# Optimization experiments

Measured on AMD Instinct MI355X. Metric: run time of the kernel, lower is better.

The kernel has to match this reference:

```python
import jax, jax.numpy as jnp
import numpy as np

H = 128      # hidden_channels
G = 512      # number of graphs in the batch
NEG_SLOPE = 0.2


def _seg_sum(x, idx, n):
    return jax.ops.segment_sum(x, idx, num_segments=n)


def _sage(x_src, x_dst, ei, Wl, bl, Wr):
    # PyG SAGEConv: lin_l(mean_j x_j) + lin_r(x_i); lin_l has bias, lin_r does not.
    s, d = ei[0], ei[1]
    n = x_dst.shape[0]
    agg = _seg_sum(x_src[s], d, n)
    cnt = _seg_sum(jnp.ones((ei.shape[1],), x_src.dtype), d, n)
    mean = agg / jnp.maximum(cnt, 1.0)[:, None]
    return mean @ Wl + bl + x_dst @ Wr


def _gat(x_src, x_dst, ei, Ws, Wd, a_s, a_d, b):
    # PyG GATConv (heads=1, add_self_loops=False, bipartite): segment softmax over dst.
    s, d = ei[0], ei[1]
    n = x_dst.shape[0]
    hs = x_src @ Ws                                  # [N_src, H]
    hd = x_dst @ Wd                                  # [N_dst, H]
    logit = jax.nn.leaky_relu((hs @ a_s)[s] + (hd @ a_d)[d], NEG_SLOPE)
    m = jax.ops.segment_max(logit, d, num_segments=n)
    e = jnp.exp(logit - m[d])
    z = _seg_sum(e, d, n)
    alpha = e / jnp.maximum(z[d], 1e-16)
    return _seg_sum(alpha[:, None] * hs[s], d, n) + b


def _gcn(x, ei, W, b):
    # PyG GCNConv with add_self_loops=True, normalize=True (same src/dst node type).
    s, d = ei[0], ei[1]
    n = x.shape[0]
    deg = _seg_sum(jnp.ones((ei.shape[1],), x.dtype), d, n) + 1.0  # +1 self loop
    dis = jax.lax.rsqrt(deg)
    h = x @ W
    norm = dis[s] * dis[d]
    out = _seg_sum(norm[:, None] * h[s], d, n) + (dis * dis)[:, None] * h
    return out + b


def _pool(x, b):
    s = _seg_sum(x, b, G)
    c = _seg_sum(jnp.ones((x.shape[0],), x.dtype), b, G)
    return s / jnp.maximum(c, 1.0)[:, None]


def setup_inputs() -> dict:
    key = jax.random.key(0)
    ks = iter(jax.random.split(key, 80))
    scale = 1.0 / np.sqrt(H)

    def nrm(shape, sc=scale):
        return jax.random.normal(next(ks), shape, jnp.float32) * sc

    def edges(e, n_src, n_dst):
        src = jax.random.randint(next(ks), (e,), 0, n_src, jnp.int32)
        dst = jax.random.randint(next(ks), (e,), 0, n_dst, jnp.int32)
        return jnp.stack([src, dst])

    def batch(n):
        return jnp.sort(jax.random.randint(next(ks), (n,), 0, G, jnp.int32))

    N_CD, N_SEQ, N_ANNO, N_RANGE, N_MD = 100000, 80000, 80000, 80000, 50000
    inp = {
        'x_cd': nrm((N_CD, H), 1.0), 'x_seq': nrm((N_SEQ, H), 1.0),
        'x_anno': nrm((N_ANNO, H), 1.0), 'x_range': nrm((N_RANGE, H), 1.0),
        'x_md': nrm((N_MD, H), 1.0),
        'ei_seq': edges(160000, N_CD, N_SEQ),
        'ei_anno': edges(200000, N_CD, N_ANNO),
        'ei_range': edges(200000, N_CD, N_RANGE),
        'ei_comp': edges(300000, N_MD, N_CD),
        'ei_cc': edges(300000, N_CD, N_CD),
        'ei_mm': edges(150000, N_MD, N_MD),
        'b_cd': batch(N_CD), 'b_seq': batch(N_SEQ), 'b_anno': batch(N_ANNO),
        'b_range': batch(N_RANGE), 'b_md': batch(N_MD),
    }
    # per-layer stacked params (leading axis = 2 layers)
    for nm, shp in [('Wsl_seq', (2, H, H)), ('bs_seq', (2, H)), ('Wsr_seq', (2, H, H)),
                    ('Wsl_anno', (2, H, H)), ('bs_anno', (2, H)), ('Wsr_anno', (2, H, H)),
                    ('Wg_comp_s', (2, H, H)), ('Wg_comp_d', (2, H, H)),
                    ('ag_comp_s', (2, H)), ('ag_comp_d', (2, H)), ('bg_comp', (2, H)),
                    ('Wg_range_s', (2, H, H)), ('Wg_range_d', (2, H, H)),
                    ('ag_range_s', (2, H)), ('ag_range_d', (2, H)), ('bg_range', (2, H)),
                    ('Wc_cc', (2, H, H)), ('bc_cc', (2, H)),
                    ('Wc_mm', (2, H, H)), ('bc_mm', (2, H)),
                    ('lin1_W', (5 * H, H)), ('lin1_b', (H,)),
                    ('lin2_W', (H, 1)), ('lin2_b', (1,))]:
        inp[nm] = nrm(shp)
    return inp


def reference(x_cd, x_seq, x_anno, x_range, x_md,
              ei_seq, ei_anno, ei_range, ei_comp, ei_cc, ei_mm,
              b_cd, b_seq, b_anno, b_range, b_md,
              Wsl_seq, bs_seq, Wsr_seq, Wsl_anno, bs_anno, Wsr_anno,
              Wg_comp_s, Wg_comp_d, ag_comp_s, ag_comp_d, bg_comp,
              Wg_range_s, Wg_range_d, ag_range_s, ag_range_d, bg_range,
              Wc_cc, bc_cc, Wc_mm, bc_mm,
              lin1_W, lin1_b, lin2_W, lin2_b):
    for l in range(2):
        # HeteroConv aggr='sum': CD receives GAT(MD->CD) + GCN(CD->CD)
        n_cd = (_gat(x_md, x_cd, ei_comp, Wg_comp_s[l], Wg_comp_d[l],
                     ag_comp_s[l], ag_comp_d[l], bg_comp[l])
                + _gcn(x_cd, ei_cc, Wc_cc[l], bc_cc[l]))
        n_seq = _sage(x_cd, x_seq, ei_seq, Wsl_seq[l], bs_seq[l], Wsr_seq[l])
        n_anno = _sage(x_cd, x_anno, ei_anno, Wsl_anno[l], bs_anno[l], Wsr_anno[l])
        n_range = _gat(x_cd, x_range, ei_range, Wg_range_s[l], Wg_range_d[l],
                       ag_range_s[l], ag_range_d[l], bg_range[l])
        n_md = _gcn(x_md, ei_mm, Wc_mm[l], bc_mm[l])
        x_cd, x_seq, x_anno, x_range, x_md = (
            jax.nn.relu(n_cd), jax.nn.relu(n_seq), jax.nn.relu(n_anno),
            jax.nn.relu(n_range), jax.nn.relu(n_md))
    emb = jnp.concatenate([_pool(x_cd, b_cd), _pool(x_seq, b_seq),
                           _pool(x_anno, b_anno), _pool(x_range, b_range),
                           _pool(x_md, b_md)], axis=-1)        # [G, 5H]
    h = jax.nn.relu(emb @ lin1_W + lin1_b)  # Dropout(0.7) is identity in eval
    return (h @ lin2_W + lin2_b).reshape(-1)  # [G]
```

## Files before the change

### kernel.cpp

```cpp
#include <hip/hip_runtime.h>

#define HD 128
#define GNUM 512
#define RPB 520
#define IDXCAP 512
#define TM 32

typedef __attribute__((ext_vector_type(8))) short short8v;
typedef __attribute__((ext_vector_type(4))) float f32x4;

__device__ __forceinline__ void split1(float a, short& h, short& l) {
  unsigned u = __float_as_uint(a);
  unsigned hb = (u + 0x7FFFu + ((u >> 16) & 1u)) & 0xFFFF0000u;
  h = (short)(hb >> 16);
  float rest = a - __uint_as_float(hb);
  unsigned u2 = __float_as_uint(rest);
  l = (short)((u2 + 0x7FFFu + ((u2 >> 16) & 1u)) >> 16);
}

struct WTab { const float* p[8]; };
__global__ __launch_bounds__(256) void k_split_w(WTab tab, short* __restrict__ whi,
                                                 short* __restrict__ wlo)
{
  int m = blockIdx.x >> 6;
  int i = (blockIdx.x & 63) * 256 + threadIdx.x;
  const float* W = tab.p[m >> 1] + (m & 1) * 16384;
  int k = i >> 7, n = i & 127;
  short h, l;
  split1(W[k * 128 + n], h, l);
  whi[m * 16384 + n * 128 + k] = h;
  wlo[m * 16384 + n * 128 + k] = l;
}

struct COp {
  const float* A; const short* WH; const short* WL;
  const int* grp; const int* gcol;
  const float* wsrc; const float* rowsc; int mode;
};
#define CF_LD 132
__global__ __launch_bounds__(256) void k_gemm_conv(
    COp o0, COp o1, int hasO1,
    float* __restrict__ C, const float* __restrict__ bias, const float* __restrict__ bias2,
    int N, int relu,
    const float* __restrict__ avec, float* __restrict__ adot,
    const float* __restrict__ avec2, float* __restrict__ adot2,
    const int* __restrict__ bvec, float* __restrict__ poolbuf, int coloff)
{
  __shared__ char smem[TM * 136 * 2 * 2];
  __shared__ int idxbuf[IDXCAP];
  __shared__ float wbuf[IDXCAP];
  __shared__ int bsh[TM];
  short* Ah = (short*)smem;
  short* Al = Ah + TM * 136;
  float* Cf = (float*)smem;

  const int t = threadIdx.x;
  const int row0 = blockIdx.x * TM;
  const int lane = t & 63, wid = t >> 6;
  const int g = lane >> 4, cn = lane & 15;
  const int colbase = wid * 32;

  f32x4 zero = {0.f, 0.f, 0.f, 0.f};
  f32x4 acc[2][2];
#pragma unroll
  for (int rt = 0; rt < 2; ++rt) { acc[rt][0] = zero; acc[rt][1] = zero; }

  auto storeAhl = [&](int row, int ln, float4 s) {
    short4 h, l;
    split1(s.x, h.x, l.x); split1(s.y, h.y, l.y);
    split1(s.z, h.z, l.z); split1(s.w, h.w, l.w);
    *(short4*)(Ah + row * 136 + ln * 4) = h;
    *(short4*)(Al + row * 136 + ln * 4) = l;
  };

  auto stageA = [&](const float* __restrict__ A) {
#pragma unroll
    for (int i = 0; i < 4; ++i) {
      int f4 = t + i * 256;
      int row = f4 >> 5, c4 = f4 & 31;
      float4 v = make_float4(0.f, 0.f, 0.f, 0.f);
      if (row0 + row < N) v = ((const float4*)(A + (size_t)row0 * 128))[f4];
      storeAhl(row, c4, v);
    }
  };

  auto prefetch = [&](const COp& op) {
    const int row_end = min(row0 + TM, N);
    const int e_lo = op.grp[row0];
    const int cnt = min(op.grp[row_end] - e_lo, IDXCAP);
    for (int k = t; k < cnt; k += 256) {
      int idx = op.gcol[e_lo + k];
      idxbuf[k] = idx;
      if (op.wsrc) wbuf[k] = op.wsrc[idx];
    }
  };

  auto stage_gather = [&](const COp& op) {
    const int e_lo = op.grp[row0];
    const int mode = op.mode;
    const float* X = op.A;
    auto getcw = [&](int e, int& c, float& w) {
      int off = e - e_lo;
      if (off < IDXCAP) { c = idxbuf[off]; w = wbuf[off]; }
      else { c = op.gcol[e]; w = op.wsrc ? op.wsrc[c] : 0.f; }
    };
#pragma unroll
    for (int i = 0; i < 8; ++i) {
      int f = t + i * 256;
      int row = f >> 6;
      int ln = f & 31;
      int half = (f >> 5) & 1;
      int r = row0 + row;
      float4 s = make_float4(0.f, 0.f, 0.f, 0.f);
      int e0 = 0, e1 = 0;
      float rs = 0.f;
      if (r < N) {
        e0 = op.grp[r]; e1 = op.grp[r + 1];
        if (mode >= 2) rs = op.rowsc[r];
      }
      float z = 0.f;
      if (mode == 2 && half == 0 && r < N) {
        float4 xs_ = *(const float4*)(X + (size_t)r * 128 + ln * 4);
        float rr = rs * rs;
        s.x = rr * xs_.x; s.y = rr * xs_.y; s.z = rr * xs_.z; s.w = rr * xs_.w;
      }
      for (int e = e0 + half; e < e1; e += 2) {
        int c; float w;
        getcw(e, c, w);
        float p;
        if (mode == 3) {
          float v = w + rs; v = v > 0.f ? v : 0.2f * v;
          p = __expf(v); z += p;
        } else if (mode == 2) p = w * rs;
        else p = 1.f;
        float4 a = *(const float4*)(X + (size_t)c * 128 + ln * 4);
        s.x += p * a.x; s.y += p * a.y; s.z += p * a.z; s.w += p * a.w;
      }
      s.x += __shfl_xor(s.x, 32); s.y += __shfl_xor(s.y, 32);
      s.z += __shfl_xor(s.z, 32); s.w += __shfl_xor(s.w, 32);
      if (mode == 3) z += __shfl_xor(z, 32);
      if (half == 0) {
        if (mode == 1) {
          float inv = 1.f / fmaxf((float)(e1 - e0), 1.f);
          s.x *= inv; s.y *= inv; s.z *= inv; s.w *= inv;
        } else if (mode == 3) {
          float inv = (e1 > e0) ? 1.f / z : 0.f;
          s.x *= inv; s.y *= inv; s.z *= inv; s.w *= inv;
        }
        storeAhl(row, ln, s);
      }
    }
  };

  auto accum = [&](const short* __restrict__ WH, const short* __restrict__ WL) {
#pragma unroll
    for (int kg = 0; kg < 4; ++kg) {
      short8v bhi[2], blo[2];
#pragma unroll
      for (int ct = 0; ct < 2; ++ct) {
        size_t o = (size_t)(colbase + ct * 16 + cn) * 128 + kg * 32 + g * 8;
        bhi[ct] = *(const short8v*)(WH + o);
        blo[ct] = *(const short8v*)(WL + o);
      }
#pragma unroll
      for (int rt = 0; rt < 2; ++rt) {
        const int ao = (rt * 16 + cn) * 136 + kg * 32 + g * 8;
        const short8v ah = *(const short8v*)(Ah + ao);
        const short8v al = *(const short8v*)(Al + ao);
#pragma unroll
        for (int ct = 0; ct < 2; ++ct) {
          acc[rt][ct] = __builtin_amdgcn_mfma_f32_16x16x32_bf16(ah, bhi[ct], acc[rt][ct], 0, 0, 0);
          acc[rt][ct] = __builtin_amdgcn_mfma_f32_16x16x32_bf16(al, bhi[ct], acc[rt][ct], 0, 0, 0);
          acc[rt][ct] = __builtin_amdgcn_mfma_f32_16x16x32_bf16(ah, blo[ct], acc[rt][ct], 0, 0, 0);
        }
      }
    }
  };

  if (o0.mode) {
    prefetch(o0);
    __syncthreads();
    stage_gather(o0);
  } else {
    stageA(o0.A);
  }
  __syncthreads();
  if (hasO1 && o1.mode) prefetch(o1);
  accum(o0.WH, o0.WL);
  if (hasO1) {
    __syncthreads();
    if (o1.mode) stage_gather(o1); else stageA(o1.A);
    __syncthreads();
    accum(o1.WH, o1.WL);
  }
  __syncthreads();

#pragma unroll
  for (int rt = 0; rt < 2; ++rt)
#pragma unroll
    for (int ct = 0; ct < 2; ++ct)
#pragma unroll
      for (int r = 0; r < 4; ++r)
        Cf[(rt * 16 + g * 4 + r) * CF_LD + colbase + ct * 16 + cn] = acc[rt][ct][r];
  __syncthreads();

  float4* C4 = C ? (float4*)(C + (size_t)row0 * 128) : nullptr;
#pragma unroll
  for (int i = 0; i < 4; ++i) {
    int f4 = t + i * 256;
    int row = f4 >> 5, c4 = f4 & 31;
    if (row0 + row < N) {
      float4 v = *(const float4*)(Cf + row * CF_LD + c4 * 4);
      if (bias) {
        float4 bv = *(const float4*)(bias + c4 * 4);
        v.x += bv.x; v.y += bv.y; v.z += bv.z; v.w += bv.w;
      }
      if (bias2) {
        float4 bv = *(const float4*)(bias2 + c4 * 4);
        v.x += bv.x; v.y += bv.y; v.z += bv.z; v.w += bv.w;
      }
      if (relu) {
        v.x = fmaxf(v.x, 0.f); v.y = fmaxf(v.y, 0.f);
        v.z = fmaxf(v.z, 0.f); v.w = fmaxf(v.w, 0.f);
      }
      if (C) C4[f4] = v;
      *(float4*)(Cf + row * CF_LD + c4 * 4) = v;
      if (avec) {
        float4 av = *(const float4*)(avec + c4 * 4);
        float p = v.x * av.x + v.y * av.y + v.z * av.z + v.w * av.w;
#pragma unroll
        for (int o = 1; o < 32; o <<= 1) p += __shfl_xor(p, o);
        if (c4 == 0) adot[row0 + row] = p;
      }
      if (avec2) {
        float4 av = *(const float4*)(avec2 + c4 * 4);
        float p = v.x * av.x + v.y * av.y + v.z * av.z + v.w * av.w;
#pragma unroll
        for (int o = 1; o < 32; o <<= 1) p += __shfl_xor(p, o);
        if (c4 == 0) adot2[row0 + row] = p;
      }
    }
  }

  if (poolbuf) {
    if (t < TM) { int r = row0 + t; bsh[t] = (r < N) ? bvec[r] : -1; }
    __syncthreads();
    if (t < 128) {
      int c = t;
      float sum = 0.f;
      int cur = bsh[0];
      for (int r = 0; r < TM; ++r) {
        int gg = bsh[r];
        if (gg < 0) break;
        if (gg != cur) {
          atomicAdd(poolbuf + (size_t)cur * 640 + coloff + c, sum);
          sum = 0.f; cur = gg;
        }
        sum += Cf[r * CF_LD + c];
      }
      if (cur >= 0) atomicAdd(poolbuf + (size_t)cur * 640 + coloff + c, sum);
    }
  }
}

__global__ void k_rowdot(const float* __restrict__ x, const float* __restrict__ a,
                         float* __restrict__ out, int N)
{
  int wid = blockIdx.x * 4 + (threadIdx.x >> 6);
  int lane = threadIdx.x & 63;
  if (wid >= N) return;
  float2 xv = ((const float2*)x)[(size_t)wid * 64 + lane];
  float2 av = ((const float2*)a)[lane];
  float v = fmaf(xv.y, av.y, xv.x * av.x);
#pragma unroll
  for (int o = 32; o > 0; o >>= 1) v += __shfl_down(v, o);
  if (lane == 0) out[wid] = v;
}

__global__ void k_rowdot2(const float* __restrict__ x, const float* __restrict__ a1,
                          const float* __restrict__ a2, float* __restrict__ o1,
                          float* __restrict__ o2, int N)
{
  int wid = blockIdx.x * 4 + (threadIdx.x >> 6);
  int lane = threadIdx.x & 63;
  if (wid >= N) return;
  float2 xv = ((const float2*)x)[(size_t)wid * 64 + lane];
  float2 av1 = ((const float2*)a1)[lane];
  float2 av2 = ((const float2*)a2)[lane];
  float v1 = fmaf(xv.y, av1.y, xv.x * av1.x);
  float v2 = fmaf(xv.y, av2.y, xv.x * av2.x);
#pragma unroll
  for (int o = 32; o > 0; o >>= 1) { v1 += __shfl_down(v1, o); v2 += __shfl_down(v2, o); }
  if (lane == 0) { o1[wid] = v1; o2[wid] = v2; }
}

struct MTab { const float* W[8]; const float* a[8]; };
__global__ __launch_bounds__(128) void k_matvec8(MTab tb, float* __restrict__ wv)
{
  __shared__ float as[128];
  int m = blockIdx.x, i = threadIdx.x;
  as[i] = tb.a[m][i];
  __syncthreads();
  const float* W = tb.W[m];
  float v = 0.f;
  for (int j = 0; j < 128; ++j) v = fmaf(W[i * 128 + j], as[j], v);
  wv[m * 128 + i] = v;
}

struct HTab { const int* key[6]; int* cnt[6]; unsigned short* rank[6]; int bo[7]; int n[6]; };
__global__ void k_hist_rank_all(HTab tb) {
  int bi = blockIdx.x, ty = 0;
  while (ty < 5 && bi >= tb.bo[ty + 1]) ++ty;
  int i = (bi - tb.bo[ty]) * 256 + threadIdx.x;
  if (i < tb.n[ty])
    tb.rank[ty][i] = (unsigned short)atomicAdd(&tb.cnt[ty][tb.key[ty][i]], 1);
}

struct FTab { const int* es[6]; const int* ed[6]; const int* rp[6];
              const unsigned short* rank[6]; int* col[6]; int bo[7]; int n[6]; };
__global__ void k_fill_all(FTab tb) {
  int bi = blockIdx.x, ty = 0;
  while (ty < 5 && bi >= tb.bo[ty + 1]) ++ty;
  int e = (bi - tb.bo[ty]) * 256 + threadIdx.x;
  if (e >= tb.n[ty]) return;
  int p = tb.rp[ty][tb.ed[ty][e]] + (int)tb.rank[ty][e];
  tb.col[ty][p] = tb.es[ty][e];
}

struct STab { int* rp[6]; int* bs[6]; int n[6]; int bo[7]; };

__global__ __launch_bounds__(256) void k_scan_partial_all(STab tb) {
  __shared__ int red[256];
  int bi = blockIdx.x, ty = 0;
  while (ty < 5 && bi >= tb.bo[ty + 1]) ++ty;
  int lb = bi - tb.bo[ty];
  const int* rp = tb.rp[ty];
  const int N = tb.n[ty];
  const int t = threadIdx.x, base = lb * 4096;
  int s = 0;
  for (int i = t; i < 4096; i += 256) {
    int idx = base + i;
    if (idx < N) s += rp[idx];
  }
  red[t] = s;
  __syncthreads();
  for (int ofs = 128; ofs > 0; ofs >>= 1) {
    if (t < ofs) red[t] += red[t + ofs];
    __syncthreads();
  }
  if (t == 0) tb.bs[ty][lb] = red[0];
}

__global__ __launch_bounds__(256) void k_scan_bsums_all(STab tb) {
  __shared__ int sh[256];
  const int ty = blockIdx.x;
  const int nb = (tb.n[ty] + 4095) / 4096;
  const int t = threadIdx.x;
  int v = (t < nb) ? tb.bs[ty][t] : 0;
  sh[t] = v;
  __syncthreads();
  for (int ofs = 1; ofs < 256; ofs <<= 1) {
    int u = (t >= ofs) ? sh[t - ofs] : 0;
    __syncthreads();
    sh[t] += u;
    __syncthreads();
  }
  if (t < nb) tb.bs[ty][t] = sh[t] - v;
  if (t == 255) tb.rp[ty][tb.n[ty]] = sh[255];
}

__global__ __launch_bounds__(256) void k_scan_final_all(STab tb) {
  __shared__ int sh[4096 + 256];
  __shared__ int tsum[256];
  int bi = blockIdx.x, ty = 0;
  while (ty < 5 && bi >= tb.bo[ty + 1]) ++ty;
  int lb = bi - tb.bo[ty];
  int* rp = tb.rp[ty];
  const int N = tb.n[ty];
  const int t = threadIdx.x, base = lb * 4096;
  auto mp = [](int i) { return i + (i >> 4); };
#pragma unroll
  for (int i = 0; i < 16; ++i) {
    int idx = base + i * 256 + t;
    sh[mp(i * 256 + t)] = (idx < N) ? rp[idx] : 0;
  }
  __syncthreads();
  int s = 0;
#pragma unroll
  for (int j = 0; j < 16; ++j) s += sh[mp(t * 16 + j)];
  tsum[t] = s;
  __syncthreads();
  for (int ofs = 1; ofs < 256; ofs <<= 1) {
    int u = (t >= ofs) ? tsum[t - ofs] : 0;
    __syncthreads();
    tsum[t] += u;
    __syncthreads();
  }
  int pre = tsum[t] - s + tb.bs[ty][lb];
#pragma unroll
  for (int j = 0; j < 16; ++j) {
    int v = sh[mp(t * 16 + j)];
    sh[mp(t * 16 + j)] = pre;
    pre += v;
  }
  __syncthreads();
#pragma unroll
  for (int i = 0; i < 16; ++i) {
    int idx = base + i * 256 + t;
    if (idx < N) rp[idx] = sh[mp(i * 256 + t)];
  }
}

struct BTab { const int* b[5]; int n[5]; };
__global__ __launch_bounds__(512) void k_runptr(BTab tb, int* __restrict__ rpb_all) {
  const int ty = blockIdx.x;
  const int* b = tb.b[ty];
  const int N = tb.n[ty];
  const int t = threadIdx.x;
  int lo = 0, hi = N;
  while (lo < hi) {
    int mid = (lo + hi) >> 1;
    if (b[mid] < t) lo = mid + 1; else hi = mid;
  }
  rpb_all[ty * RPB + t] = lo;
  if (t == 0) rpb_all[ty * RPB + GNUM] = N;
}

struct DTab { const int* rp[2]; float* dis[2]; int n[2]; int bo[3]; };
__global__ void k_dis2(DTab tb) {
  int bi = blockIdx.x, ty = (bi >= tb.bo[1]) ? 1 : 0;
  int n = (bi - tb.bo[ty]) * 256 + threadIdx.x;
  if (n < tb.n[ty]) tb.dis[ty][n] = rsqrtf((float)(tb.rp[ty][n + 1] - tb.rp[ty][n]) + 1.f);
}

__global__ void k_mlp(const float* __restrict__ pool, const int* __restrict__ rpb_all,
                      const float* __restrict__ W1, const float* __restrict__ b1,
                      const float* __restrict__ W2, const float* __restrict__ b2,
                      float* __restrict__ out)
{
  __shared__ float emb[640];
  __shared__ float red[128];
  const int g = blockIdx.x, t = threadIdx.x;
  for (int i = t; i < 640; i += 128) {
    int type = i >> 7;
    int cnt = rpb_all[type * RPB + g + 1] - rpb_all[type * RPB + g];
    emb[i] = pool[(size_t)g * 640 + i] / fmaxf((float)cnt, 1.f);
  }
  __syncthreads();
  float acc = b1[t];
  for (int i = 0; i < 640; ++i) acc = fmaf(emb[i], W1[i * 128 + t], acc);
  float h = fmaxf(acc, 0.f);
  red[t] = h * W2[t];
  __syncthreads();
  for (int s = 64; s > 0; s >>= 1) {
    if (t < s) red[t] += red[t + s];
    __syncthreads();
  }
  if (t == 0) out[g] = red[0] + b2[0];
}

extern "C" void kernel_launch(void* const* d_in, const int* in_sizes, int n_in,
                              void* d_out, int out_size, void* d_ws, size_t ws_size,
                              hipStream_t stream)
{
  auto fin = [&](int i) { return (const float*)d_in[i]; };
  auto iin = [&](int i) { return (const int*)d_in[i]; };

  const float *x_cd = fin(0), *x_seq = fin(1), *x_anno = fin(2), *x_range = fin(3), *x_md = fin(4);
  const int *ei_seq = iin(5), *ei_anno = iin(6), *ei_range = iin(7),
            *ei_comp = iin(8), *ei_cc = iin(9), *ei_mm = iin(10);
  const int *b_cd = iin(11), *b_seq = iin(12), *b_anno = iin(13), *b_range = iin(14), *b_md = iin(15);

  const int N_CD = in_sizes[0] / HD, N_SEQ = in_sizes[1] / HD, N_ANNO = in_sizes[2] / HD,
            N_RANGE = in_sizes[3] / HD, N_MD = in_sizes[4] / HD;
  const int E_seq = in_sizes[5] / 2, E_anno = in_sizes[6] / 2, E_range = in_sizes[7] / 2,
            E_comp = in_sizes[8] / 2, E_cc = in_sizes[9] / 2, E_mm = in_sizes[10] / 2;
  const int N_OTH = max(max(N_SEQ, N_ANNO), N_RANGE);

  auto WLm = [&](int i, int l) { return fin(i) + (size_t)l * HD * HD; };
  auto WLv = [&](int i, int l) { return fin(i) + (size_t)l * HD; };

  float* ws = (float*)d_ws;
  size_t off = 0;
  auto alloc = [&](size_t n) { float* p = ws + off; off += (n + 3) & ~(size_t)3; return p; };
  float* xcd1 = alloc((size_t)N_CD * HD);
  float* xmd1 = alloc((size_t)N_MD * HD);
  float* xoth = alloc((size_t)N_OTH * HD);
  float* t1   = alloc((size_t)N_CD * HD);
  float* sA = alloc((size_t)N_CD);
  float* sB = alloc((size_t)N_CD);
  float* sC = alloc((size_t)N_CD);
  float* sD = alloc((size_t)N_CD);
  float* sE = alloc((size_t)N_CD);
  float* sF = alloc((size_t)N_CD);
  float* dis_cc = alloc((size_t)N_CD);
  float* dis_mm = alloc((size_t)N_MD);
  float* wv8 = alloc(8 * HD);
  float* pool = alloc((size_t)GNUM * 5 * HD);
  short* whi = (short*)(ws + off); off += (size_t)16 * 16384 / 2;
  short* wlo = (short*)(ws + off); off += (size_t)16 * 16384 / 2;
  auto alloci = [&](size_t n) { int* p = (int*)(ws + off); off += (n + 3) & ~(size_t)3; return p; };
  int* bsall = alloci(6 * 256);
  int* rpb_all = alloci(5 * RPB);
  int Nds[6] = {N_SEQ, N_ANNO, N_RANGE, N_CD, N_CD, N_MD};
  int Es[6]  = {E_seq, E_anno, E_range, E_comp, E_cc, E_mm};
  int* rps[6];
  int* rp0 = alloci(0);
  { size_t tot = 0; for (int i = 0; i < 6; ++i) tot += (size_t)Nds[i] + 1;
    int* p = alloci(tot); rp0 = p;
    for (int i = 0; i < 6; ++i) { rps[i] = p; p += Nds[i] + 1; } }
  size_t rp_tot_bytes = 0; for (int i = 0; i < 6; ++i) rp_tot_bytes += ((size_t)Nds[i] + 1) * 4;
  unsigned short* ranks[6];
  for (int i = 0; i < 6; ++i) ranks[i] = (unsigned short*)alloci(((size_t)Es[i] + 1) / 2);
  int* cols[6];  for (int i = 0; i < 6; ++i) cols[i] = alloci((size_t)Es[i]);
  (void)n_in;

  if (off * sizeof(float) > ws_size) {
    hipMemsetAsync(d_out, 0, (size_t)out_size * sizeof(float), stream);
    return;
  }

  auto ew = [&](size_t elems) { return dim3((unsigned)((elems + 255) / 256)); };
  auto nw = [&](int N) { return dim3((unsigned)((N + 3) / 4)); };

  hipMemsetAsync(pool, 0, (size_t)GNUM * 5 * HD * sizeof(float), stream);

  WTab tab;
  tab.p[0] = fin(16); tab.p[1] = fin(18); tab.p[2] = fin(19); tab.p[3] = fin(21);
  tab.p[4] = fin(22); tab.p[5] = fin(27); tab.p[6] = fin(32); tab.p[7] = fin(34);
  k_split_w<<<dim3(1024), dim3(256), 0, stream>>>(tab, whi, wlo);

  MTab mt;
  mt.W[0] = WLm(22, 0); mt.a[0] = WLv(24, 0);
  mt.W[1] = WLm(23, 0); mt.a[1] = WLv(25, 0);
  mt.W[2] = WLm(22, 1); mt.a[2] = WLv(24, 1);
  mt.W[3] = WLm(23, 1); mt.a[3] = WLv(25, 1);
  mt.W[4] = WLm(27, 0); mt.a[4] = WLv(29, 0);
  mt.W[5] = WLm(28, 0); mt.a[5] = WLv(30, 0);
  mt.W[6] = WLm(27, 1); mt.a[6] = WLv(29, 1);
  mt.W[7] = WLm(28, 1); mt.a[7] = WLv(30, 1);
  k_matvec8<<<dim3(8), dim3(128), 0, stream>>>(mt, wv8);

  k_rowdot<<<nw(N_MD), dim3(256), 0, stream>>>(x_md, wv8 + 0 * 128, sA, N_MD);
  k_rowdot2<<<nw(N_CD), dim3(256), 0, stream>>>(x_cd, wv8 + 1 * 128, wv8 + 4 * 128,
                                                sB, sC, N_CD);
  k_rowdot<<<nw(N_RANGE), dim3(256), 0, stream>>>(x_range, wv8 + 5 * 128, sD, N_RANGE);

  {
    BTab bt;
    bt.b[0] = b_cd; bt.n[0] = N_CD;  bt.b[1] = b_seq; bt.n[1] = N_SEQ;
    bt.b[2] = b_anno; bt.n[2] = N_ANNO;  bt.b[3] = b_range; bt.n[3] = N_RANGE;
    bt.b[4] = b_md; bt.n[4] = N_MD;
    k_runptr<<<dim3(5), dim3(512), 0, stream>>>(bt, rpb_all);
  }

  const int* ess[6] = {ei_seq, ei_anno, ei_range, ei_comp, ei_cc, ei_mm};
  const int* eds[6] = {ei_seq + E_seq, ei_anno + E_anno, ei_range + E_range,
                       ei_comp + E_comp, ei_cc + E_cc, ei_mm + E_mm};
  hipMemsetAsync(rp0, 0, rp_tot_bytes, stream);
  {
    HTab ht; int b = 0;
    for (int i = 0; i < 6; ++i) {
      ht.key[i] = eds[i]; ht.cnt[i] = rps[i]; ht.rank[i] = ranks[i];
      ht.bo[i] = b; b += (Es[i] + 255) / 256; ht.n[i] = Es[i];
    }
    ht.bo[6] = b;
    k_hist_rank_all<<<dim3(b), dim3(256), 0, stream>>>(ht);
  }
  {
    STab st; int b = 0;
    for (int i = 0; i < 6; ++i) {
      st.rp[i] = rps[i]; st.bs[i] = bsall + i * 256;
      st.n[i] = Nds[i]; st.bo[i] = b; b += (Nds[i] + 4095) / 4096;
    }
    st.bo[6] = b;
    k_scan_partial_all<<<dim3(b), dim3(256), 0, stream>>>(st);
    k_scan_bsums_all<<<dim3(6), dim3(256), 0, stream>>>(st);
    k_scan_final_all<<<dim3(b), dim3(256), 0, stream>>>(st);
  }
  {
    FTab ft; int b = 0;
    for (int i = 0; i < 6; ++i) {
      ft.es[i] = ess[i]; ft.ed[i] = eds[i]; ft.rp[i] = rps[i]; ft.rank[i] = ranks[i];
      ft.col[i] = cols[i]; ft.bo[i] = b; b += (Es[i] + 255) / 256; ft.n[i] = Es[i];
    }
    ft.bo[6] = b;
    k_fill_all<<<dim3(b), dim3(256), 0, stream>>>(ft);
  }
  int *rp_seq = rps[0], *rp_anno = rps[1], *rp_range = rps[2],
      *rp_comp = rps[3], *rp_cc = rps[4], *rp_mm = rps[5];
  int *col_seq = cols[0], *col_anno = cols[1], *col_range = cols[2],
      *col_comp = cols[3], *col_cc = cols[4], *col_mm = cols[5];
  {
    DTab dt;
    dt.rp[0] = rp_cc; dt.dis[0] = dis_cc; dt.n[0] = N_CD;
    dt.rp[1] = rp_mm; dt.dis[1] = dis_mm; dt.n[1] = N_MD;
    dt.bo[0] = 0; dt.bo[1] = (N_CD + 255) / 256;
    dt.bo[2] = dt.bo[1] + (N_MD + 255) / 256;
    k_dis2<<<dim3(dt.bo[2]), dim3(256), 0, stream>>>(dt);
  }

  auto WHp = [&](int sidx, int layer) { return whi + (size_t)(sidx * 2 + layer) * 16384; };
  auto WLp = [&](int sidx, int layer) { return wlo + (size_t)(sidx * 2 + layer) * 16384; };

  auto mkop = [&](int mode, const float* A, int sidx, int layer,
                  const int* grp, const int* gcol,
                  const float* wsrc, const float* rowsc) {
    COp o;
    o.A = A; o.WH = WHp(sidx, layer); o.WL = WLp(sidx, layer);
    o.grp = grp; o.gcol = gcol; o.wsrc = wsrc; o.rowsc = rowsc; o.mode = mode;
    return o;
  };
  auto launch = [&](COp o0, COp o1, int hasO1, float* C, const float* bias,
                    const float* bias2, int N, int relu,
                    const float* avec, float* adot, const float* avec2, float* adot2,
                    const int* bvec, int coloff) {
    k_gemm_conv<<<dim3((N + TM - 1) / TM), dim3(256), 0, stream>>>(
        o0, o1, hasO1, C, bias, bias2, N, relu, avec, adot, avec2, adot2,
        bvec, bvec ? pool : nullptr, coloff);
  };
  COp nop = {};

  launch(mkop(3, x_md, 4, 0, rp_comp, col_comp, sA, sB),
         mkop(2, x_cd, 6, 0, rp_cc, col_cc, dis_cc, dis_cc), 1,
         xcd1, WLv(26, 0), WLv(33, 0), N_CD, 1,
         wv8 + 3 * 128, sB, wv8 + 6 * 128, sE, nullptr, 0);
  launch(mkop(2, x_md, 7, 0, rp_mm, col_mm, dis_mm, dis_mm), nop, 0,
         xmd1, WLv(35, 0), nullptr, N_MD, 1,
         wv8 + 2 * 128, sA, nullptr, nullptr, nullptr, 0);
  launch(mkop(3, xmd1, 4, 1, rp_comp, col_comp, sA, sB),
         mkop(2, xcd1, 6, 1, rp_cc, col_cc, dis_cc, dis_cc), 1,
         nullptr, WLv(26, 1), WLv(33, 1), N_CD, 1,
         nullptr, nullptr, nullptr, nullptr, b_cd, 0 * HD);
  launch(mkop(2, xmd1, 7, 1, rp_mm, col_mm, dis_mm, dis_mm), nop, 0,
         nullptr, WLv(35, 1), nullptr, N_MD, 1,
         nullptr, nullptr, nullptr, nullptr, b_md, 4 * HD);

  launch(mkop(1, x_cd, 0, 0, rp_seq, col_seq, nullptr, nullptr),
         mkop(0, x_seq, 1, 0, nullptr, nullptr, nullptr, nullptr), 1,
         xoth, WLv(17, 0), nullptr, N_SEQ, 1,
         nullptr, nullptr, nullptr, nullptr, nullptr, 0);
  launch(mkop(1, xcd1, 0, 1, rp_seq, col_seq, nullptr, nullptr),
         mkop(0, xoth, 1, 1, nullptr, nullptr, nullptr, nullptr), 1,
         nullptr, WLv(17, 1), nullptr, N_SEQ, 1,
         nullptr, nullptr, nullptr, nullptr, b_seq, 1 * HD);
  launch(mkop(1, x_cd, 2, 0, rp_anno, col_anno, nullptr, nullptr),
         mkop(0, x_anno, 3, 0, nullptr, nullptr, nullptr, nullptr), 1,
         t1, WLv(20, 0), nullptr, N_ANNO, 1,
         nullptr, nullptr, nullptr, nullptr, nullptr, 0);
  launch(mkop(1, xcd1, 2, 1, rp_anno, col_anno, nullptr, nullptr),
         mkop(0, t1, 3, 1, nullptr, nullptr, nullptr, nullptr), 1,
         nullptr, WLv(20, 1), nullptr, N_ANNO, 1,
         nullptr, nullptr, nullptr, nullptr, b_anno, 2 * HD);
  launch(mkop(3, x_cd, 5, 0, rp_range, col_range, sC, sD), nop, 0,
         xoth, WLv(31, 0), nullptr, N_RANGE, 1,
         wv8 + 7 * 128, sF, nullptr, nullptr, nullptr, 0);
  launch(mkop(3, xcd1, 5, 1, rp_range, col_range, sE, sF), nop, 0,
         nullptr, WLv(31, 1), nullptr, N_RANGE, 1,
         nullptr, nullptr, nullptr, nullptr, b_range, 3 * HD);

  k_mlp<<<dim3(GNUM), dim3(128), 0, stream>>>(
      pool, rpb_all, fin(36), fin(37), fin(38), fin(39), (float*)d_out);
}
```

Measured before the change: 921.3 us.

## Parallelize gather-aggregation over edges with shared-memory atomics instead of per-row loops

Replaces the per-row edge loop in the fused gather+GEMM kernel with an edge-parallel pass. Each block maps its edges to local rows with a binary search over cached row pointers, then accumulates weighted neighbor features into a shared fp32 buffer using LDS atomics. Normalization and any overflow edges beyond the index cache are handled afterwards. This aims to fix load imbalance from skewed degrees, at the cost of extra LDS (about 17KB more per block, which may reduce occupancy), atomic contention, extra barriers and nondeterministic summation order.

```diff
diff --git a/kernel.cpp b/kernel.cpp
--- a/kernel.cpp
+++ b/kernel.cpp
@@ -47,8 +47,13 @@
     const int* __restrict__ bvec, float* __restrict__ poolbuf, int coloff)
 {
   __shared__ char smem[TM * 136 * 2 * 2];
+  __shared__ float accumbuf[TM * CF_LD];
   __shared__ int idxbuf[IDXCAP];
   __shared__ float wbuf[IDXCAP];
+  __shared__ unsigned char rowof[IDXCAP];
+  __shared__ int rpsh[TM + 1];
+  __shared__ float rssh[TM];
+  __shared__ float zsh[TM];
   __shared__ int bsh[TM];
   short* Ah = (short*)smem;
   short* Al = Ah + TM * 136;
@@ -84,62 +89,91 @@
     }
   };
 
-  auto prefetch = [&](const COp& op) {
-    const int row_end = min(row0 + TM, N);
-    const int e_lo = op.grp[row0];
-    const int cnt = min(op.grp[row_end] - e_lo, IDXCAP);
+  auto prefA = [&](const COp& op) {
+    if (t <= TM) rpsh[t] = op.grp[min(row0 + t, N)];
+    if (op.mode >= 2 && t < TM && row0 + t < N) rssh[t] = op.rowsc[row0 + t];
+  };
+
+  auto prefB = [&](const COp& op) {
+    const int e_lo = rpsh[0];
+    const int cnt = min(rpsh[TM] - e_lo, IDXCAP);
     for (int k = t; k < cnt; k += 256) {
       int idx = op.gcol[e_lo + k];
       idxbuf[k] = idx;
       if (op.wsrc) wbuf[k] = op.wsrc[idx];
-    }
-  };
-
-  auto stage_gather = [&](const COp& op) {
-    const int e_lo = op.grp[row0];
+      int lo = 0, hi = TM;
+      while (lo + 1 < hi) {
+        int mid = (lo + hi) >> 1;
+        if (rpsh[mid] <= e_lo + k) lo = mid; else hi = mid;
+      }
+      rowof[k] = (unsigned char)lo;
+    }
+    for (int k = t; k < TM * CF_LD; k += 256) accumbuf[k] = 0.f;
+    if (t < TM) zsh[t] = 0.f;
+  };
+
+  auto edgepass = [&](const COp& op) {
+    const int cnt = min(rpsh[TM] - rpsh[0], IDXCAP);
     const int mode = op.mode;
     const float* X = op.A;
-    auto getcw = [&](int e, int& c, float& w) {
-      int off = e - e_lo;
-      if (off < IDXCAP) { c = idxbuf[off]; w = wbuf[off]; }
-      else { c = op.gcol[e]; w = op.wsrc ? op.wsrc[c] : 0.f; }
-    };
-#pragma unroll
-    for (int i = 0; i < 8; ++i) {
-      int f = t + i * 256;
-      int row = f >> 6;
-      int ln = f & 31;
-      int half = (f >> 5) & 1;
+    const int total = cnt * 32;
+#pragma unroll 2
+    for (int base = t; base < total; base += 256) {
+      int k = base >> 5, ln = base & 31;
+      int c = idxbuf[k];
+      int row = rowof[k];
+      float p;
+      if (mode == 3) {
+        float v = wbuf[k] + rssh[row];
+        v = v > 0.f ? v : 0.2f * v;
+        p = __expf(v);
+        if (ln == 0) atomicAdd(&zsh[row], p);
+      } else if (mode == 2) {
+        p = wbuf[k] * rssh[row];
+      } else {
+        p = 1.f;
+      }
+      float4 a = *(const float4*)(X + (size_t)c * 128 + ln * 4);
+      float* dst = accumbuf + row * CF_LD + ln * 4;
+      atomicAdd(dst + 0, p * a.x);
+      atomicAdd(dst + 1, p * a.y);
+      atomicAdd(dst + 2, p * a.z);
+      atomicAdd(dst + 3, p * a.w);
+    }
+  };
+
+  auto normalize = [&](const COp& op) {
+    const int e_lo = rpsh[0];
+    const int mode = op.mode;
+    const float* X = op.A;
+#pragma unroll
+    for (int i = 0; i < 4; ++i) {
+      int f4 = t + i * 256;
+      int row = f4 >> 5, ln = f4 & 31;
       int r = row0 + row;
-      float4 s = make_float4(0.f, 0.f, 0.f, 0.f);
-      int e0 = 0, e1 = 0;
-      float rs = 0.f;
+      float4 s = *(const float4*)(accumbuf + row * CF_LD + ln * 4);
       if (r < N) {
-        e0 = op.grp[r]; e1 = op.grp[r + 1];
-        if (mode >= 2) rs = op.rowsc[r];
-      }
-      float z = 0.f;
-      if (mode == 2 && half == 0 && r < N) {
-        float4 xs_ = *(const float4*)(X + (size_t)r * 128 + ln * 4);
-        float rr = rs * rs;
-        s.x = rr * xs_.x; s.y = rr * xs_.y; s.z = rr * xs_.z; s.w = rr * xs_.w;
-      }
-      for (int e = e0 + half; e < e1; e += 2) {
-        int c; float w;
-        getcw(e, c, w);
-        float p;
-        if (mode == 3) {
-          float v = w + rs; v = v > 0.f ? v : 0.2f * v;
-          p = __expf(v); z += p;
-        } else if (mode == 2) p = w * rs;
-        else p = 1.f;
-        float4 a = *(const float4*)(X + (size_t)c * 128 + ln * 4);
-        s.x += p * a.x; s.y += p * a.y; s.z += p * a.z; s.w += p * a.w;
-      }
-      s.x += __shfl_xor(s.x, 32); s.y += __shfl_xor(s.y, 32);
-      s.z += __shfl_xor(s.z, 32); s.w += __shfl_xor(s.w, 32);
-      if (mode == 3) z += __shfl_xor(z, 32);
-      if (half == 0) {
+        int e0 = op.grp[r], e1 = op.grp[r + 1];
+        float rs = (mode >= 2) ? rssh[row] : 0.f;
+        float z = (mode == 3) ? zsh[row] : 0.f;
+        int ovf = max(e0, e_lo + IDXCAP);
+        for (int e = ovf; e < e1; ++e) {
+          int c = op.gcol[e];
+          float w = op.wsrc ? op.wsrc[c] : 0.f;
+          float p;
+          if (mode == 3) {
+            float v = w + rs; v = v > 0.f ? v : 0.2f * v;
+            p = __expf(v); z += p;
+          } else if (mode == 2) p = w * rs;
+          else p = 1.f;
+          float4 a = *(const float4*)(X + (size_t)c * 128 + ln * 4);
+          s.x += p * a.x; s.y += p * a.y; s.z += p * a.z; s.w += p * a.w;
+        }
+        if (mode == 2) {
+          float4 xs_ = *(const float4*)(X + (size_t)r * 128 + ln * 4);
+          float rr = rs * rs;
+          s.x += rr * xs_.x; s.y += rr * xs_.y; s.z += rr * xs_.z; s.w += rr * xs_.w;
+        }
         if (mode == 1) {
           float inv = 1.f / fmaxf((float)(e1 - e0), 1.f);
           s.x *= inv; s.y *= inv; s.z *= inv; s.w *= inv;
@@ -147,9 +181,19 @@
           float inv = (e1 > e0) ? 1.f / z : 0.f;
           s.x *= inv; s.y *= inv; s.z *= inv; s.w *= inv;
         }
-        storeAhl(row, ln, s);
-      }
-    }
+      }
+      storeAhl(row, ln, s);
+    }
+  };
+
+  auto gather_stage = [&](const COp& op) {
+    prefA(op);
+    __syncthreads();
+    prefB(op);
+    __syncthreads();
+    edgepass(op);
+    __syncthreads();
+    normalize(op);
   };
 
   auto accum = [&](const short* __restrict__ WH, const short* __restrict__ WL) {
@@ -177,19 +221,12 @@
     }
   };
 
-  if (o0.mode) {
-    prefetch(o0);
-    __syncthreads();
-    stage_gather(o0);
-  } else {
-    stageA(o0.A);
-  }
-  __syncthreads();
-  if (hasO1 && o1.mode) prefetch(o1);
+  if (o0.mode) gather_stage(o0); else stageA(o0.A);
+  __syncthreads();
   accum(o0.WH, o0.WL);
   if (hasO1) {
     __syncthreads();
-    if (o1.mode) stage_gather(o1); else stageA(o1.A);
+    if (o1.mode) gather_stage(o1); else stageA(o1.A);
     __syncthreads();
     accum(o1.WH, o1.WL);
   }
```

New measurement: 2.376 ms. 158% more time.

## Precompute per-edge GAT/GCN weights in CSR order and simplify gather loop

Applied to the files above, without the earlier changes.

Adds a k_edgew kernel that computes per-edge weights in CSR position: the exp of the leaky-relu logit for GAT, with softmax denominators accumulated by atomics, and the normalised dis[s]*dis[d] for GCN. The gather stage then reads the weight directly by edge position instead of recomputing the exp and the products per lane. The gather also drops the half-wave split and shuffle reduction in favour of one lane-group per row with a two-way unrolled edge loop. The cost is extra launches, per-edge weight buffers, atomics on z and a memset. Removing the split halves the parallelism per row for high-degree nodes.

```diff
diff --git a/kernel.cpp b/kernel.cpp
--- a/kernel.cpp
+++ b/kernel.cpp
@@ -89,9 +89,8 @@
     const int e_lo = op.grp[row0];
     const int cnt = min(op.grp[row_end] - e_lo, IDXCAP);
     for (int k = t; k < cnt; k += 256) {
-      int idx = op.gcol[e_lo + k];
-      idxbuf[k] = idx;
-      if (op.wsrc) wbuf[k] = op.wsrc[idx];
+      idxbuf[k] = op.gcol[e_lo + k];
+      if (op.wsrc) wbuf[k] = op.wsrc[e_lo + k];
     }
   };
 
@@ -102,14 +101,12 @@
     auto getcw = [&](int e, int& c, float& w) {
       int off = e - e_lo;
       if (off < IDXCAP) { c = idxbuf[off]; w = wbuf[off]; }
-      else { c = op.gcol[e]; w = op.wsrc ? op.wsrc[c] : 0.f; }
+      else { c = op.gcol[e]; w = op.wsrc ? op.wsrc[e] : 0.f; }
     };
 #pragma unroll
-    for (int i = 0; i < 8; ++i) {
-      int f = t + i * 256;
-      int row = f >> 6;
-      int ln = f & 31;
-      int half = (f >> 5) & 1;
+    for (int i = 0; i < 4; ++i) {
+      int f4 = t + i * 256;
+      int row = f4 >> 5, ln = f4 & 31;
       int r = row0 + row;
       float4 s = make_float4(0.f, 0.f, 0.f, 0.f);
       int e0 = 0, e1 = 0;
@@ -118,37 +115,38 @@
         e0 = op.grp[r]; e1 = op.grp[r + 1];
         if (mode >= 2) rs = op.rowsc[r];
       }
-      float z = 0.f;
-      if (mode == 2 && half == 0 && r < N) {
+      if (mode == 2 && r < N) {
         float4 xs_ = *(const float4*)(X + (size_t)r * 128 + ln * 4);
         float rr = rs * rs;
         s.x = rr * xs_.x; s.y = rr * xs_.y; s.z = rr * xs_.z; s.w = rr * xs_.w;
       }
-      for (int e = e0 + half; e < e1; e += 2) {
+      int e = e0;
+      for (; e + 1 < e1; e += 2) {
+        int c0, c1; float w0, w1;
+        getcw(e, c0, w0);
+        getcw(e + 1, c1, w1);
+        float p0 = (mode == 1) ? 1.f : w0;
+        float p1 = (mode == 1) ? 1.f : w1;
+        float4 a = *(const float4*)(X + (size_t)c0 * 128 + ln * 4);
+        float4 b = *(const float4*)(X + (size_t)c1 * 128 + ln * 4);
+        s.x += p0 * a.x + p1 * b.x; s.y += p0 * a.y + p1 * b.y;
+        s.z += p0 * a.z + p1 * b.z; s.w += p0 * a.w + p1 * b.w;
+      }
+      if (e < e1) {
         int c; float w;
         getcw(e, c, w);
-        float p;
-        if (mode == 3) {
-          float v = w + rs; v = v > 0.f ? v : 0.2f * v;
-          p = __expf(v); z += p;
-        } else if (mode == 2) p = w * rs;
-        else p = 1.f;
+        float p = (mode == 1) ? 1.f : w;
         float4 a = *(const float4*)(X + (size_t)c * 128 + ln * 4);
         s.x += p * a.x; s.y += p * a.y; s.z += p * a.z; s.w += p * a.w;
       }
-      s.x += __shfl_xor(s.x, 32); s.y += __shfl_xor(s.y, 32);
-      s.z += __shfl_xor(s.z, 32); s.w += __shfl_xor(s.w, 32);
-      if (mode == 3) z += __shfl_xor(z, 32);
-      if (half == 0) {
-        if (mode == 1) {
-          float inv = 1.f / fmaxf((float)(e1 - e0), 1.f);
-          s.x *= inv; s.y *= inv; s.z *= inv; s.w *= inv;
-        } else if (mode == 3) {
-          float inv = (e1 > e0) ? 1.f / z : 0.f;
-          s.x *= inv; s.y *= inv; s.z *= inv; s.w *= inv;
-        }
-        storeAhl(row, ln, s);
-      }
+      if (mode == 1) {
+        float inv = 1.f / fmaxf((float)(e1 - e0), 1.f);
+        s.x *= inv; s.y *= inv; s.z *= inv; s.w *= inv;
+      } else if (mode == 3) {
+        float inv = (e1 > e0) ? 1.f / rs : 0.f;
+        s.x *= inv; s.y *= inv; s.z *= inv; s.w *= inv;
+      }
+      storeAhl(row, ln, s);
     }
   };
 
@@ -261,6 +259,31 @@
       if (cur >= 0) atomicAdd(poolbuf + (size_t)cur * 640 + coloff + c, sum);
     }
   }
+}
+
+struct ETab {
+  const int* es[4]; const int* ed[4]; const int* rp[4];
+  const unsigned short* rank[4];
+  float* wexp[4]; const float* s_[4]; const float* d_[4]; float* z[4];
+  int isgat[4]; int bo[5]; int n[4];
+};
+__global__ void k_edgew(ETab tb) {
+  int bi = blockIdx.x, ty = 0;
+  while (ty < 3 && bi >= tb.bo[ty + 1]) ++ty;
+  int e = (bi - tb.bo[ty]) * 256 + threadIdx.x;
+  if (e >= tb.n[ty]) return;
+  int src = tb.es[ty][e], dst = tb.ed[ty][e];
+  int p = tb.rp[ty][dst] + (int)tb.rank[ty][e];
+  float w;
+  if (tb.isgat[ty]) {
+    float v = tb.s_[ty][src] + tb.d_[ty][dst];
+    v = v > 0.f ? v : 0.2f * v;
+    w = __expf(v);
+    atomicAdd(tb.z[ty] + dst, w);
+  } else {
+    w = tb.s_[ty][src] * tb.d_[ty][dst];
+  }
+  tb.wexp[ty][p] = w;
 }
 
 __global__ void k_rowdot(const float* __restrict__ x, const float* __restrict__ a,
@@ -497,6 +520,14 @@
   float* dis_mm = alloc((size_t)N_MD);
   float* wv8 = alloc(8 * HD);
   float* pool = alloc((size_t)GNUM * 5 * HD);
+  float* we_comp0 = alloc((size_t)E_comp);
+  float* we_comp1 = alloc((size_t)E_comp);
+  float* we_cc    = alloc((size_t)E_cc);
+  float* we_mm    = alloc((size_t)E_mm);
+  float* we_rng0  = alloc((size_t)E_range);
+  float* we_rng1  = alloc((size_t)E_range);
+  float* zall = alloc((size_t)2 * N_CD + 2 * N_RANGE);
+  float* zc0 = zall, *zc1 = zall + N_CD, *zr0 = zc1 + N_CD, *zr1 = zr0 + N_RANGE;
   short* whi = (short*)(ws + off); off += (size_t)16 * 16384 / 2;
   short* wlo = (short*)(ws + off); off += (size_t)16 * 16384 / 2;
   auto alloci = [&](size_t n) { int* p = (int*)(ws + off); off += (n + 3) & ~(size_t)3; return p; };
@@ -524,6 +555,7 @@
   auto nw = [&](int N) { return dim3((unsigned)((N + 3) / 4)); };
 
   hipMemsetAsync(pool, 0, (size_t)GNUM * 5 * HD * sizeof(float), stream);
+  hipMemsetAsync(zall, 0, ((size_t)2 * N_CD + 2 * N_RANGE) * sizeof(float), stream);
 
   WTab tab;
   tab.p[0] = fin(16); tab.p[1] = fin(18); tab.p[2] = fin(19); tab.p[3] = fin(21);
@@ -598,6 +630,25 @@
     dt.bo[0] = 0; dt.bo[1] = (N_CD + 255) / 256;
     dt.bo[2] = dt.bo[1] + (N_MD + 255) / 256;
     k_dis2<<<dim3(dt.bo[2]), dim3(256), 0, stream>>>(dt);
+  }
+
+  {
+    ETab et; int b = 0;
+    et.es[0] = ei_comp; et.ed[0] = ei_comp + E_comp; et.rp[0] = rp_comp;
+    et.rank[0] = ranks[3]; et.wexp[0] = we_comp0; et.s_[0] = sA; et.d_[0] = sB;
+    et.z[0] = zc0; et.isgat[0] = 1; et.n[0] = E_comp;
+    et.es[1] = ei_range; et.ed[1] = ei_range + E_range; et.rp[1] = rp_range;
+    et.rank[1] = ranks[2]; et.wexp[1] = we_rng0; et.s_[1] = sC; et.d_[1] = sD;
+    et.z[1] = zr0; et.isgat[1] = 1; et.n[1] = E_range;
+    et.es[2] = ei_cc; et.ed[2] = ei_cc + E_cc; et.rp[2] = rp_cc;
+    et.rank[2] = ranks[4]; et.wexp[2] = we_cc; et.s_[2] = dis_cc; et.d_[2] = dis_cc;
+    et.z[2] = nullptr; et.isgat[2] = 0; et.n[2] = E_cc;
+    et.es[3] = ei_mm; et.ed[3] = ei_mm + E_mm; et.rp[3] = rp_mm;
+    et.rank[3] = ranks[5]; et.wexp[3] = we_mm; et.s_[3] = dis_mm; et.d_[3] = dis_mm;
+    et.z[3] = nullptr; et.isgat[3] = 0; et.n[3] = E_mm;
+    for (int i = 0; i < 4; ++i) { et.bo[i] = b; b += (et.n[i] + 255) / 256; }
+    et.bo[4] = b;
+    k_edgew<<<dim3(b), dim3(256), 0, stream>>>(et);
   }
 
   auto WHp = [&](int sidx, int layer) { return whi + (size_t)(sidx * 2 + layer) * 16384; };
@@ -619,20 +670,32 @@
         o0, o1, hasO1, C, bias, bias2, N, relu, avec, adot, avec2, adot2,
         bvec, bvec ? pool : nullptr, coloff);
   };
+  auto edgew1 = [&](const int* es, int E, const int* rp, const unsigned short* rank,
+                    float* wexp, const float* s_, const float* d_, float* z) {
+    ETab et;
+    et.es[0] = es; et.ed[0] = es + E; et.rp[0] = rp; et.rank[0] = rank;
+    et.wexp[0] = wexp; et.s_[0] = s_; et.d_[0] = d_; et.z[0] = z;
+    et.isgat[0] = 1; et.n[0] = E;
+    et.bo[0] = 0; et.bo[1] = (E + 255) / 256; et.bo[2] = et.bo[1];
+    et.bo[3] = et.bo[1]; et.bo[4] = et.bo[1];
+    et.n[1] = et.n[2] = et.n[3] = 0;
+    k_edgew<<<dim3(et.bo[1]), dim3(256), 0, stream>>>(et);
+  };
   COp nop = {};
 
-  launch(mkop(3, x_md, 4, 0, rp_comp, col_comp, sA, sB),
-         mkop(2, x_cd, 6, 0, rp_cc, col_cc, dis_cc, dis_cc), 1,
+  launch(mkop(3, x_md, 4, 0, rp_comp, col_comp, we_comp0, zc0),
+         mkop(2, x_cd, 6, 0, rp_cc, col_cc, we_cc, dis_cc), 1,
          xcd1, WLv(26, 0), WLv(33, 0), N_CD, 1,
          wv8 + 3 * 128, sB, wv8 + 6 * 128, sE, nullptr, 0);
-  launch(mkop(2, x_md, 7, 0, rp_mm, col_mm, dis_mm, dis_mm), nop, 0,
+  launch(mkop(2, x_md, 7, 0, rp_mm, col_mm, we_mm, dis_mm), nop, 0,
          xmd1, WLv(35, 0), nullptr, N_MD, 1,
          wv8 + 2 * 128, sA, nullptr, nullptr, nullptr, 0);
-  launch(mkop(3, xmd1, 4, 1, rp_comp, col_comp, sA, sB),
-         mkop(2, xcd1, 6, 1, rp_cc, col_cc, dis_cc, dis_cc), 1,
+  edgew1(ei_comp, E_comp, rp_comp, ranks[3], we_comp1, sA, sB, zc1);
+  launch(mkop(3, xmd1, 4, 1, rp_comp, col_comp, we_comp1, zc1),
+         mkop(2, xcd1, 6, 1, rp_cc, col_cc, we_cc, dis_cc), 1,
          nullptr, WLv(26, 1), WLv(33, 1), N_CD, 1,
          nullptr, nullptr, nullptr, nullptr, b_cd, 0 * HD);
-  launch(mkop(2, xmd1, 7, 1, rp_mm, col_mm, dis_mm, dis_mm), nop, 0,
+  launch(mkop(2, xmd1, 7, 1, rp_mm, col_mm, we_mm, dis_mm), nop, 0,
          nullptr, WLv(35, 1), nullptr, N_MD, 1,
          nullptr, nullptr, nullptr, nullptr, b_md, 4 * HD);
 
@@ -652,10 +715,11 @@
          mkop(0, t1, 3, 1, nullptr, nullptr, nullptr, nullptr), 1,
          nullptr, WLv(20, 1), nullptr, N_ANNO, 1,
          nullptr, nullptr, nullptr, nullptr, b_anno, 2 * HD);
-  launch(mkop(3, x_cd, 5, 0, rp_range, col_range, sC, sD), nop, 0,
+  launch(mkop(3, x_cd, 5, 0, rp_range, col_range, we_rng0, zr0), nop, 0,
          xoth, WLv(31, 0), nullptr, N_RANGE, 1,
          wv8 + 7 * 128, sF, nullptr, nullptr, nullptr, 0);
-  launch(mkop(3, xcd1, 5, 1, rp_range, col_range, sE, sF), nop, 0,
+  edgew1(ei_range, E_range, rp_range, ranks[2], we_rng1, sE, sF, zr1);
+  launch(mkop(3, xcd1, 5, 1, rp_range, col_range, we_rng1, zr1), nop, 0,
          nullptr, WLv(31, 1), nullptr, N_RANGE, 1,
          nullptr, nullptr, nullptr, nullptr, b_range, 3 * HD);
 
```

After: 916.6 us. Within noise of the previous version (-0.5%).
